# Performance work log

Hardware: AMD Instinct MI355X
Metric: run time of the kernel (lower is better)

## Reference

```python
import jax, jax.numpy as jnp
import numpy as np

B, N, D, H = 4, 2048, 768, 12
HD = D // H  # head_dim = 64


def setup_inputs() -> dict:
    key = jax.random.key(0)
    k1, k2, k3 = jax.random.split(key, 3)
    z = jax.random.normal(k1, (B, N, D), dtype=jnp.float32)
    # per-head qkv Linear weights, torch Linear convention: y = x @ W.T + b
    Wqkv = jax.random.normal(k2, (H, 3 * HD, D), dtype=jnp.float32) * 0.02
    bqkv = jnp.zeros((H, 3 * HD), dtype=jnp.float32)
    Wmsa = jax.random.normal(k3, (D, D), dtype=jnp.float32) * 0.02
    bmsa = jnp.zeros((D,), dtype=jnp.float32)
    return {"z": z, "Wqkv": Wqkv, "bqkv": bqkv, "Wmsa": Wmsa, "bmsa": bmsa}


def reference(z, Wqkv, bqkv, Wmsa, bmsa):
    # All heads' qkv projections in one einsum: [B,N,D] x [H,3hd,D] -> [B,H,N,3hd]
    qkv = jnp.einsum("bnd,hed->bhne", z, Wqkv) + bqkv[None, :, None, :]
    q, k, v = jnp.split(qkv, 3, axis=-1)  # each [B,H,N,hd]
    scale = 1.0 / jnp.sqrt(jnp.asarray(HD, dtype=z.dtype))
    scores = jnp.einsum("bhqd,bhkd->bhqk", q, k) * scale  # [B,H,N,N]
    attn = jax.nn.softmax(scores, axis=-1)
    out = jnp.einsum("bhqk,bhkd->bhqd", attn, v)  # [B,H,N,hd]
    # concat heads (head order matches the torch per-head cat)
    out = out.transpose(0, 2, 1, 3).reshape(B, N, H * HD)  # [B,N,D]
    return out @ Wmsa.T + bmsa
```

## Files before the change

kernel.cpp:

```cpp
#include <hip/hip_runtime.h>

typedef unsigned short u16;
typedef unsigned int u32;
typedef __attribute__((ext_vector_type(8))) short bf16x8;
typedef __attribute__((ext_vector_type(4))) float f32x4;

#define B_ 4
#define H_ 12
#define N_ 2048
#define D_ 768
#define HD_ 64
#define NTOK (B_ * N_)
#define NE   (H_ * 3 * HD_)

#define BK 64
#define CPITCH 144

#define QSCALE 0.18033688011112042f

__device__ __forceinline__ u16 f2bf(float f) {
    u32 u = __float_as_uint(f);
    u += 0x7fffu + ((u >> 16) & 1u);
    return (u16)(u >> 16);
}

__device__ __forceinline__ f32x4 mfma16(bf16x8 a, bf16x8 b, f32x4 c) {
    return __builtin_amdgcn_mfma_f32_16x16x32_bf16(a, b, c, 0, 0, 0);
}

__device__ __forceinline__ void g2l16(const u16* g, u16* l) {
    __builtin_amdgcn_global_load_lds(
        (const __attribute__((address_space(1))) void*)g,
        (__attribute__((address_space(3))) void*)l, 16, 0, 0);
}

#define NZ4  (NTOK * D_ / 4)
#define NWQ4 (NE * D_ / 4)
#define NWM4 (D_ * D_ / 4)
__global__ __launch_bounds__(256) void cvt_all(const float* __restrict__ z,
                                               const float* __restrict__ Wq,
                                               const float* __restrict__ Wm,
                                               u16* __restrict__ Xbf,
                                               u16* __restrict__ Wqb,
                                               u16* __restrict__ Wmb) {
    int i = blockIdx.x * blockDim.x + threadIdx.x;
    const float* src;
    u16* dst;
    int j;
    if (i < NZ4) {
        src = z; dst = Xbf; j = i;
    } else if (i < NZ4 + NWQ4) {
        src = Wq; dst = Wqb; j = i - NZ4;
    } else if (i < NZ4 + NWQ4 + NWM4) {
        src = Wm; dst = Wmb; j = i - NZ4 - NWQ4;
    } else {
        return;
    }
    float4 v = ((const float4*)src)[j];
    u32 lo = (u32)f2bf(v.x) | ((u32)f2bf(v.y) << 16);
    u32 hi = (u32)f2bf(v.z) | ((u32)f2bf(v.w) << 16);
    ((uint2*)dst)[j] = make_uint2(lo, hi);
}

#define GEMM_CORE(Xp, Wp, TM, SMELEMS)                                         \
    __shared__ u16 smem[SMELEMS];                                              \
    u16* ldsA = smem;                                                          \
    u16* ldsB = smem + (TM) * BK;                                              \
    const int tid = threadIdx.x;                                               \
    const int wave = tid >> 6, lane = tid & 63;                                \
    const int lrow = lane & 15, quad = lane >> 4;                              \
    const int mbase = blockIdx.x * (TM);                                       \
    const int nbase = blockIdx.y * 128;                                        \
    const int srow = tid >> 3;                                      \
    const int schunk = tid & 7;                                                \
    const int sk = (schunk ^ (srow & 7)) << 3;   \
    const int sdst = srow * BK + schunk * 8;     \
    const u16* gA = Xp + (size_t)(mbase + srow) * D_ + sk;                     \
    const u16* gB = Wp + (size_t)(nbase + srow) * D_ + sk;                     \
    const int m_ofs = (wave >> 1) * ((TM) / 2);                                \
    const int n_ofs = (wave & 1) * 64;                                         \
    const int e_ = lrow & 7;                                                   \
    const int offA0 = (m_ofs + lrow) * BK + ((quad ^ e_) << 3);                \
    const int offB0 = (n_ofs + lrow) * BK + ((quad ^ e_) << 3);                \
    f32x4 acc[(TM) / 32][4] = {};                                              \
    for (int kt = 0; kt < D_; kt += BK) {                                      \
        __syncthreads();                                                       \
        _Pragma("unroll") for (int i = 0; i < (TM) / 32; i++)                  \
            g2l16(gA + (size_t)(32 * i) * D_ + kt, ldsA + sdst + i * 32 * BK); \
        _Pragma("unroll") for (int i = 0; i < 4; i++)                          \
            g2l16(gB + (size_t)(32 * i) * D_ + kt, ldsB + sdst + i * 32 * BK); \
        __syncthreads();                                                       \
        _Pragma("unroll") for (int ks = 0; ks < 2; ks++) {                     \
            const int oa = offA0 ^ (ks << 5);                                  \
            const int ob = offB0 ^ (ks << 5);                                  \
            bf16x8 af[(TM) / 32], bfr[4];                                      \
            _Pragma("unroll") for (int c = 0; c < (TM) / 32; c++)              \
                af[c] = *(const bf16x8*)&ldsA[oa + c * 16 * BK];               \
            _Pragma("unroll") for (int c = 0; c < 4; c++)                      \
                bfr[c] = *(const bf16x8*)&ldsB[ob + c * 16 * BK];              \
            _Pragma("unroll") for (int i = 0; i < (TM) / 32; i++)              \
                _Pragma("unroll") for (int j = 0; j < 4; j++)                  \
                    acc[i][j] = mfma16(af[i], bfr[j], acc[i][j]);              \
        }                                                                      \
    }

__global__ __launch_bounds__(256) void gemm_qkv(const u16* __restrict__ X,
                                                const u16* __restrict__ W,
                                                const float* __restrict__ bqkv,
                                                u16* __restrict__ Qs,
                                                u16* __restrict__ Ks,
                                                u16* __restrict__ Vt) {
    GEMM_CORE(X, W, 128, 128 * CPITCH)
    __syncthreads();
    u16* ldsC = smem;
#pragma unroll
    for (int cn = 0; cn < 4; cn++) {
        const int E = nbase + n_ofs + cn * 16;
        const int h = E / 192;
        const int rr = E - h * 192;
        const int kind = rr >> 6;
        const float bias = bqkv[E + lrow];
        if (kind == 2) {
            const int d = (rr & 63) + lrow;
#pragma unroll
            for (int cm = 0; cm < 4; cm++) {
                const int t0 = mbase + m_ofs + cm * 16 + quad * 4;
                const int b_ = t0 >> 11, n0 = t0 & (N_ - 1);
                const size_t bh = (size_t)(b_ * H_ + h);
                uint2 pk;
                pk.x = (u32)f2bf(acc[cm][cn][0] + bias) |
                       ((u32)f2bf(acc[cm][cn][1] + bias) << 16);
                pk.y = (u32)f2bf(acc[cm][cn][2] + bias) |
                       ((u32)f2bf(acc[cm][cn][3] + bias) << 16);
                *(uint2*)&Vt[(bh * HD_ + d) * N_ + n0] = pk;
            }
        } else {
            const int fcol = n_ofs + cn * 16 + lrow;
            const float scale = (kind == 0) ? QSCALE : 1.0f;
#pragma unroll
            for (int cm = 0; cm < 4; cm++)
#pragma unroll
                for (int r = 0; r < 4; r++) {
                    const int tok = m_ofs + cm * 16 + quad * 4 + r;
                    ldsC[tok * CPITCH + fcol] =
                        f2bf((acc[cm][cn][r] + bias) * scale);
                }
        }
    }
    __syncthreads();
    {
        const int tok = tid >> 1, fh = tid & 1;
        const int gf = nbase + fh * 64;
        const int kind2 = (gf >> 6) % 3;
        if (kind2 != 2) {
            const int h2 = gf / 192;
            const int t = mbase + tok;
            const int b2 = t >> 11, n2 = t & (N_ - 1);
            u16* dst = (kind2 == 0 ? Qs : Ks) +
                       ((size_t)(b2 * H_ + h2) * N_ + n2) * HD_;
            const u16* src = &ldsC[tok * CPITCH + fh * 64];
#pragma unroll
            for (int j = 0; j < 8; j++)
                *(uint4*)&dst[j * 8] = *(const uint4*)&src[j * 8];
        }
    }
}

__global__ __launch_bounds__(256) void gemm_out(const u16* __restrict__ X2,
                                                const u16* __restrict__ W,
                                                const float* __restrict__ bmsa,
                                                float* __restrict__ out) {
    GEMM_CORE(X2, W, 64, (64 + 128) * BK)
#pragma unroll
    for (int cn = 0; cn < 4; cn++) {
        const int col = nbase + n_ofs + cn * 16 + lrow;
        const float bias = bmsa[col];
#pragma unroll
        for (int cm = 0; cm < 2; cm++) {
#pragma unroll
            for (int r = 0; r < 4; r++) {
                const int t = mbase + m_ofs + cm * 16 + quad * 4 + r;
                out[(size_t)t * D_ + col] = acc[cm][cn][r] + bias;
            }
        }
    }
}

__global__ __launch_bounds__(256, 3) void flash_attn(const u16* __restrict__ Qs,
                                                     const u16* __restrict__ Ks,
                                                     const u16* __restrict__ Vt,
                                                     u16* __restrict__ X2) {
    __shared__ u16 ldsK[2][64 * HD_];
    __shared__ u16 ldsV[2][64 * HD_];
    __shared__ u16 ldsP[4][2][16][68];
    const int tid = threadIdx.x;
    const int wave = tid >> 6, lane = tid & 63;
    const int lrow = lane & 15, quad = lane >> 4;
    const int qbase = blockIdx.x * 128 + wave * 32;
    const int bh = blockIdx.y;
    const int b = bh / H_, h = bh - b * H_;

    const u16* Kb = Ks + (size_t)bh * N_ * HD_;
    const u16* Vb = Vt + (size_t)bh * HD_ * N_;

    const int srow = tid >> 3;
    const int schunk = tid & 7;
    const int skk = (schunk ^ (srow & 7)) << 3;
    const int sdst = srow * HD_ + schunk * 8;

    bf16x8 qa[2][2];
#pragma unroll
    for (int t = 0; t < 2; t++) {
        const u16* Qb = Qs + ((size_t)bh * N_ + qbase + t * 16 + lrow) * HD_ + quad * 8;
        qa[t][0] = *(const bf16x8*)(Qb);
        qa[t][1] = *(const bf16x8*)(Qb + 32);
    }

    const int fofs = (quad ^ (lrow & 7)) << 3;
    const short onebf = (short)0x3F80;
    const bf16x8 ones = {onebf, onebf, onebf, onebf, onebf, onebf, onebf, onebf};

    f32x4 Oacc[2][4] = {};
    f32x4 lacc[2] = {};

    {
        const u16* gK = Kb + (size_t)srow * HD_ + skk;
        g2l16(gK, &ldsK[0][sdst]);
        g2l16(gK + (size_t)32 * HD_, &ldsK[0][sdst + 32 * HD_]);
        const u16* gV = Vb + (size_t)srow * N_ + skk;
        g2l16(gV, &ldsV[0][sdst]);
        g2l16(gV + (size_t)32 * N_, &ldsV[0][sdst + 32 * HD_]);
    }

    for (int it = 0; it < N_ / 64; it++) {
        const int cur = it & 1;
        __syncthreads();
        if (it + 1 < N_ / 64) {
            const int kt2 = (it + 1) << 6;
            const u16* gK = Kb + (size_t)(kt2 + srow) * HD_ + skk;
            g2l16(gK, &ldsK[cur ^ 1][sdst]);
            g2l16(gK + (size_t)32 * HD_, &ldsK[cur ^ 1][sdst + 32 * HD_]);
            const u16* gV = Vb + (size_t)srow * N_ + kt2 + skk;
            g2l16(gV, &ldsV[cur ^ 1][sdst]);
            g2l16(gV + (size_t)32 * N_, &ldsV[cur ^ 1][sdst + 32 * HD_]);
        }
        bf16x8 kf[8];
#pragma unroll
        for (int c = 0; c < 4; c++) {
            const int o = (c * 16 + lrow) * HD_ + fofs;
            kf[2 * c]     = *(const bf16x8*)&ldsK[cur][o];
            kf[2 * c + 1] = *(const bf16x8*)&ldsK[cur][o ^ 32];
        }
        f32x4 s[2][4] = {};
#pragma unroll
        for (int t = 0; t < 2; t++)
#pragma unroll
            for (int c = 0; c < 4; c++) {
                s[t][c] = mfma16(kf[2 * c], qa[t][0], s[t][c]);
                s[t][c] = mfma16(kf[2 * c + 1], qa[t][1], s[t][c]);
            }
#pragma unroll
        for (int t = 0; t < 2; t++)
#pragma unroll
            for (int c = 0; c < 4; c++) {
                u32 a0 = __float_as_uint(__builtin_amdgcn_exp2f(s[t][c][0])) + 0x8000u;
                u32 a1 = __float_as_uint(__builtin_amdgcn_exp2f(s[t][c][1])) + 0x8000u;
                u32 a2 = __float_as_uint(__builtin_amdgcn_exp2f(s[t][c][2])) + 0x8000u;
                u32 a3 = __float_as_uint(__builtin_amdgcn_exp2f(s[t][c][3])) + 0x8000u;
                uint2 pk;
                pk.x = __builtin_amdgcn_perm(a1, a0, 0x07060302u);
                pk.y = __builtin_amdgcn_perm(a3, a2, 0x07060302u);
                *(uint2*)&ldsP[wave][t][lrow][c * 16 + quad * 4] = pk;
            }
        bf16x8 pa[2][2];
#pragma unroll
        for (int t = 0; t < 2; t++) {
            pa[t][0] = *(const bf16x8*)&ldsP[wave][t][lrow][quad * 8];
            pa[t][1] = *(const bf16x8*)&ldsP[wave][t][lrow][32 + quad * 8];
        }
#pragma unroll
        for (int t = 0; t < 2; t++) {
            lacc[t] = mfma16(pa[t][0], ones, lacc[t]);
            lacc[t] = mfma16(pa[t][1], ones, lacc[t]);
        }
#pragma unroll
        for (int c = 0; c < 4; c++) {
            const int o = (c * 16 + lrow) * HD_ + fofs;
            bf16x8 v0 = *(const bf16x8*)&ldsV[cur][o];
            bf16x8 v1 = *(const bf16x8*)&ldsV[cur][o ^ 32];
#pragma unroll
            for (int t = 0; t < 2; t++) {
                Oacc[t][c] = mfma16(pa[t][0], v0, Oacc[t][c]);
                Oacc[t][c] = mfma16(pa[t][1], v1, Oacc[t][c]);
            }
        }
    }
#pragma unroll
    for (int t = 0; t < 2; t++)
#pragma unroll
        for (int r = 0; r < 4; r++) {
            const float inv = 1.0f / lacc[t][r];
            const int qrow = qbase + t * 16 + quad * 4 + r;
#pragma unroll
            for (int c = 0; c < 4; c++) {
                X2[((size_t)b * N_ + qrow) * D_ + h * HD_ + c * 16 + lrow] =
                    f2bf(Oacc[t][c][r] * inv);
            }
        }
}

extern "C" void kernel_launch(void* const* d_in, const int* in_sizes, int n_in,
                              void* d_out, int out_size, void* d_ws, size_t ws_size,
                              hipStream_t stream) {
    const float* z    = (const float*)d_in[0];
    const float* Wqkv = (const float*)d_in[1];
    const float* bqkv = (const float*)d_in[2];
    const float* Wmsa = (const float*)d_in[3];
    const float* bmsa = (const float*)d_in[4];
    float* out = (float*)d_out;

    u16* Xbf = (u16*)d_ws;
    u16* Wqb = Xbf + (size_t)NTOK * D_;
    u16* Wmb = Wqb + (size_t)NE * D_;
    u16* Qs  = Wmb + (size_t)D_ * D_;
    u16* Ks  = Qs + (size_t)B_ * H_ * N_ * HD_;
    u16* Vt  = Ks + (size_t)B_ * H_ * N_ * HD_;
    u16* X2  = Vt + (size_t)B_ * H_ * N_ * HD_;

    const int ntot = NZ4 + NWQ4 + NWM4;
    cvt_all<<<(ntot + 255) / 256, 256, 0, stream>>>(z, Wqkv, Wmsa, Xbf, Wqb, Wmb);

    gemm_qkv<<<dim3(NTOK / 128, NE / 128), 256, 0, stream>>>(Xbf, Wqb, bqkv, Qs, Ks, Vt);
    flash_attn<<<dim3(N_ / 128, B_ * H_), 256, 0, stream>>>(Qs, Ks, Vt, X2);
    gemm_out<<<dim3(NTOK / 64, D_ / 128), 256, 0, stream>>>(X2, Wmb, bmsa, out);
}
```

Before: 215.3 us.

## Double-buffer GEMM LDS tiles, shrink QKV tile to 64 rows, truncate P

Both GEMMs now use ping-pong LDS buffers so the next K-tile is loaded while the current one is multiplied, with one barrier per iteration instead of two. The QKV projection switches to 64-row tiles with a doubled grid, and its epilogue copy is spread over four threads per token. In attention, the bf16 conversion of softmax probabilities drops the rounding add and truncates instead. The goals are hiding global load latency and improving occupancy and parallelism, at the cost of more LDS per block and slightly less precise probabilities.

After: 208.6 us. -3.1%, faster.

```diff
diff --git a/kernel.cpp b/kernel.cpp
--- a/kernel.cpp
+++ b/kernel.cpp
@@ -64,8 +64,8 @@
 
 #define GEMM_CORE(Xp, Wp, TM, SMELEMS)                                         \
     __shared__ u16 smem[SMELEMS];                                              \
-    u16* ldsA = smem;                                                          \
-    u16* ldsB = smem + (TM) * BK;                                              \
+    u16* ldsA = smem;                                          \
+    u16* ldsB = smem + 2 * (TM) * BK;                         \
     const int tid = threadIdx.x;                                               \
     const int wave = tid >> 6, lane = tid & 63;                                \
     const int lrow = lane & 15, quad = lane >> 4;                              \
@@ -83,16 +83,27 @@
     const int offA0 = (m_ofs + lrow) * BK + ((quad ^ e_) << 3);                \
     const int offB0 = (n_ofs + lrow) * BK + ((quad ^ e_) << 3);                \
     f32x4 acc[(TM) / 32][4] = {};                                              \
-    for (int kt = 0; kt < D_; kt += BK) {                                      \
-        __syncthreads();                                                       \
-        _Pragma("unroll") for (int i = 0; i < (TM) / 32; i++)                  \
-            g2l16(gA + (size_t)(32 * i) * D_ + kt, ldsA + sdst + i * 32 * BK); \
-        _Pragma("unroll") for (int i = 0; i < 4; i++)                          \
-            g2l16(gB + (size_t)(32 * i) * D_ + kt, ldsB + sdst + i * 32 * BK); \
-        __syncthreads();                                                       \
+    _Pragma("unroll") for (int i = 0; i < (TM) / 32; i++)                      \
+        g2l16(gA + (size_t)(32 * i) * D_, ldsA + sdst + i * 32 * BK);          \
+    _Pragma("unroll") for (int i = 0; i < 4; i++)                              \
+        g2l16(gB + (size_t)(32 * i) * D_, ldsB + sdst + i * 32 * BK);          \
+    for (int it = 0; it < D_ / BK; it++) {                                     \
+        const int cur = it & 1;                                                \
+        const int abase = cur * (TM) * BK, bbase = cur * 128 * BK;             \
+        __syncthreads();   \
+        if (it + 1 < D_ / BK) {                                                \
+            const int kt2 = (it + 1) * BK;                                     \
+            const int nb = cur ^ 1;                                            \
+            _Pragma("unroll") for (int i = 0; i < (TM) / 32; i++)              \
+                g2l16(gA + (size_t)(32 * i) * D_ + kt2,                        \
+                      ldsA + nb * (TM) * BK + sdst + i * 32 * BK);             \
+            _Pragma("unroll") for (int i = 0; i < 4; i++)                      \
+                g2l16(gB + (size_t)(32 * i) * D_ + kt2,                        \
+                      ldsB + nb * 128 * BK + sdst + i * 32 * BK);              \
+        }                                                                      \
         _Pragma("unroll") for (int ks = 0; ks < 2; ks++) {                     \
-            const int oa = offA0 ^ (ks << 5);                                  \
-            const int ob = offB0 ^ (ks << 5);                                  \
+            const int oa = abase + (offA0 ^ (ks << 5));                        \
+            const int ob = bbase + (offB0 ^ (ks << 5));                        \
             bf16x8 af[(TM) / 32], bfr[4];                                      \
             _Pragma("unroll") for (int c = 0; c < (TM) / 32; c++)              \
                 af[c] = *(const bf16x8*)&ldsA[oa + c * 16 * BK];               \
@@ -110,7 +121,7 @@
                                                 u16* __restrict__ Qs,
                                                 u16* __restrict__ Ks,
                                                 u16* __restrict__ Vt) {
-    GEMM_CORE(X, W, 128, 128 * CPITCH)
+    GEMM_CORE(X, W, 64, 24576)
     __syncthreads();
     u16* ldsC = smem;
 #pragma unroll
@@ -123,7 +134,7 @@
         if (kind == 2) {
             const int d = (rr & 63) + lrow;
 #pragma unroll
-            for (int cm = 0; cm < 4; cm++) {
+            for (int cm = 0; cm < 2; cm++) {
                 const int t0 = mbase + m_ofs + cm * 16 + quad * 4;
                 const int b_ = t0 >> 11, n0 = t0 & (N_ - 1);
                 const size_t bh = (size_t)(b_ * H_ + h);
@@ -138,7 +149,7 @@
             const int fcol = n_ofs + cn * 16 + lrow;
             const float scale = (kind == 0) ? QSCALE : 1.0f;
 #pragma unroll
-            for (int cm = 0; cm < 4; cm++)
+            for (int cm = 0; cm < 2; cm++)
 #pragma unroll
                 for (int r = 0; r < 4; r++) {
                     const int tok = m_ofs + cm * 16 + quad * 4 + r;
@@ -149,7 +160,8 @@
     }
     __syncthreads();
     {
-        const int tok = tid >> 1, fh = tid & 1;
+        const int tok = tid >> 2, sub = tid & 3;
+        const int fh = sub >> 1, jh = sub & 1;
         const int gf = nbase + fh * 64;
         const int kind2 = (gf >> 6) % 3;
         if (kind2 != 2) {
@@ -160,8 +172,9 @@
                        ((size_t)(b2 * H_ + h2) * N_ + n2) * HD_;
             const u16* src = &ldsC[tok * CPITCH + fh * 64];
 #pragma unroll
-            for (int j = 0; j < 8; j++)
-                *(uint4*)&dst[j * 8] = *(const uint4*)&src[j * 8];
+            for (int j = 0; j < 4; j++)
+                *(uint4*)&dst[(jh * 4 + j) * 8] =
+                    *(const uint4*)&src[(jh * 4 + j) * 8];
         }
     }
 }
@@ -170,7 +183,7 @@
                                                 const u16* __restrict__ W,
                                                 const float* __restrict__ bmsa,
                                                 float* __restrict__ out) {
-    GEMM_CORE(X2, W, 64, (64 + 128) * BK)
+    GEMM_CORE(X2, W, 64, 24576)
 #pragma unroll
     for (int cn = 0; cn < 4; cn++) {
         const int col = nbase + n_ofs + cn * 16 + lrow;
@@ -263,13 +276,13 @@
         for (int t = 0; t < 2; t++)
 #pragma unroll
             for (int c = 0; c < 4; c++) {
-                u32 a0 = __float_as_uint(__builtin_amdgcn_exp2f(s[t][c][0])) + 0x8000u;
-                u32 a1 = __float_as_uint(__builtin_amdgcn_exp2f(s[t][c][1])) + 0x8000u;
-                u32 a2 = __float_as_uint(__builtin_amdgcn_exp2f(s[t][c][2])) + 0x8000u;
-                u32 a3 = __float_as_uint(__builtin_amdgcn_exp2f(s[t][c][3])) + 0x8000u;
+                u32 b0 = __float_as_uint(__builtin_amdgcn_exp2f(s[t][c][0]));
+                u32 b1 = __float_as_uint(__builtin_amdgcn_exp2f(s[t][c][1]));
+                u32 b2 = __float_as_uint(__builtin_amdgcn_exp2f(s[t][c][2]));
+                u32 b3 = __float_as_uint(__builtin_amdgcn_exp2f(s[t][c][3]));
                 uint2 pk;
-                pk.x = __builtin_amdgcn_perm(a1, a0, 0x07060302u);
-                pk.y = __builtin_amdgcn_perm(a3, a2, 0x07060302u);
+                pk.x = __builtin_amdgcn_perm(b1, b0, 0x07060302u);
+                pk.y = __builtin_amdgcn_perm(b3, b2, 0x07060302u);
                 *(uint2*)&ldsP[wave][t][lrow][c * 16 + quad * 4] = pk;
             }
         bf16x8 pa[2][2];
@@ -330,7 +343,7 @@
     const int ntot = NZ4 + NWQ4 + NWM4;
     cvt_all<<<(ntot + 255) / 256, 256, 0, stream>>>(z, Wqkv, Wmsa, Xbf, Wqb, Wmb);
 
-    gemm_qkv<<<dim3(NTOK / 128, NE / 128), 256, 0, stream>>>(Xbf, Wqb, bqkv, Qs, Ks, Vt);
+    gemm_qkv<<<dim3(NTOK / 64, NE / 128), 256, 0, stream>>>(Xbf, Wqb, bqkv, Qs, Ks, Vt);
     flash_attn<<<dim3(N_ / 128, B_ * H_), 256, 0, stream>>>(Qs, Ks, Vt, X2);
     gemm_out<<<dim3(NTOK / 64, D_ / 128), 256, 0, stream>>>(X2, Wmb, bmsa, out);
 }
```
